# Optimization experiments

Measured on AMD Instinct MI355X. Metric: run time of the kernel, lower is better.

Reference implementation:

```python
import jax, jax.numpy as jnp
import numpy as np

B, M_IN, M_OUT, C = 4, 16, 32, 32


def setup_inputs() -> dict:
    key = jax.random.key(0)
    kx, = jax.random.split(key, 1)
    x = jax.random.normal(kx, (B, M_IN, C, C, C, C), dtype=jnp.float32)
    init = jnp.ones((M_IN, M_OUT), dtype=jnp.float32) / M_IN
    return {"x": x, "alpha": init, "beta": init, "gamma": init, "delta": init}


def reference(x, alpha, beta, gamma, delta):
    # Faithful to the torch code's permute+sum bookkeeping (note: torch's
    # permute(0,1,3,2,4,5).sum((2,4,5)) reduces ORIGINAL axes (3,4,5),
    # keeping original axis 2 -- identical to s1).
    s1 = x.sum(axis=(3, 4, 5))  # (B, M_in, C), keeps axis 2
    s2 = x.sum(axis=(3, 4, 5))  # same as s1 (permuted-sum in torch keeps axis 2)
    s3 = x.sum(axis=(2, 4, 5))  # keeps axis 3
    s4 = x.sum(axis=(2, 3, 5))  # keeps axis 4
    s = jnp.stack([s1, s2, s3, s4], axis=2)            # (B, M_in, 4, C)
    w = jnp.stack([alpha, beta, gamma, delta], axis=2)  # (M_in, M_out, 4)
    # 'bmic,mnd->bnic': sums over m and w's stack axis d; keeps s's stack axis i.
    out = jnp.einsum('bmic,mnd->bnic', s, w)            # (B, M_out, 4, C)
    return out
```

## Files before the change

### kernel.cpp

```cpp
#include <hip/hip_runtime.h>


__global__ __launch_bounds__(256) void reduce_k(const float* __restrict__ x,
                                                float* __restrict__ s3part,
                                                float* __restrict__ s4part) {
    const int t   = threadIdx.x;
    const int bid = blockIdx.x;
    const int wv  = t >> 6;
    const int g   = (t & 63) >> 3;

    __shared__ float lds3[32][33];

    const float4* xv = (const float4*)x + (size_t)bid * 8192;

    float acc4 = 0.0f;
    #pragma unroll 4
    for (int it = 0; it < 32; ++it) {
        float4 v = xv[it * 256 + t];
        float s = (v.x + v.y) + (v.z + v.w);
        s += __shfl_xor(s, 1, 64);
        s += __shfl_xor(s, 2, 64);
        s += __shfl_xor(s, 4, 64);
        acc4 += s;
        if ((t & 7) == 0) lds3[it][wv * 8 + g] = s;
    }

    if ((t & 7) == 0) s4part[bid * 32 + (t >> 3)] = acc4;

    __syncthreads();

    if (t < 32) {
        float a = 0.0f;
        #pragma unroll
        for (int k = 0; k < 32; ++k) a += lds3[t][k];
        s3part[bid * 32 + t] = a;
    }
}

__global__ __launch_bounds__(256) void finalize_k(const float* __restrict__ s3part,
                                                  const float* __restrict__ s4part,
                                                  const float* __restrict__ alpha,
                                                  const float* __restrict__ beta,
                                                  const float* __restrict__ gamma,
                                                  const float* __restrict__ delta,
                                                  float* __restrict__ out) {
    const int b = blockIdx.x;
    const int t = threadIdx.x;

    __shared__ float S1[16][32];
    __shared__ float S3[16][32];
    __shared__ float S4[16][32];
    __shared__ float W[16][32];

    #pragma unroll
    for (int i = t; i < 512; i += 256)
        W[i >> 5][i & 31] = alpha[i] + beta[i] + gamma[i] + delta[i];

    #pragma unroll
    for (int idx = t; idx < 512; idx += 256) {
        const int m = idx >> 5;
        const int c = idx & 31;
        const int bm = b * 16 + m;
        float a3 = 0.0f, a4 = 0.0f;
        #pragma unroll 4
        for (int c2 = 0; c2 < 32; ++c2) {
            a3 += s3part[(bm * 32 + c2) * 32 + c];
            a4 += s4part[(bm * 32 + c2) * 32 + c];
        }
        S3[m][c] = a3;
        S4[m][c] = a4;
        float a1 = 0.0f;
        #pragma unroll 4
        for (int k = 0; k < 32; ++k)
            a1 += s3part[(bm * 32 + c) * 32 + k];
        S1[m][c] = a1;
    }
    __syncthreads();

    #pragma unroll
    for (int idx = t; idx < 4096; idx += 256) {
        const int c = idx & 31;
        const int i = (idx >> 5) & 3;
        const int n = idx >> 7;
        const float (*S)[32] = (i <= 1) ? S1 : (i == 2 ? S3 : S4);
        float acc = 0.0f;
        #pragma unroll
        for (int m = 0; m < 16; ++m)
            acc += S[m][c] * W[m][n];
        out[((b * 32 + n) * 4 + i) * 32 + c] = acc;
    }
}

extern "C" void kernel_launch(void* const* d_in, const int* in_sizes, int n_in,
                              void* d_out, int out_size, void* d_ws, size_t ws_size,
                              hipStream_t stream) {
    const float* x     = (const float*)d_in[0];
    const float* alpha = (const float*)d_in[1];
    const float* beta  = (const float*)d_in[2];
    const float* gamma = (const float*)d_in[3];
    const float* delta = (const float*)d_in[4];
    float* out = (float*)d_out;
    float* ws  = (float*)d_ws;

    float* s3part = ws;
    float* s4part = ws + 65536;

    reduce_k<<<2048, 256, 0, stream>>>(x, s3part, s4part);
    finalize_k<<<4, 256, 0, stream>>>(s3part, s4part, alpha, beta, gamma, delta, out);
}
```

Baseline: 372.6 us.

## Replace per-iteration shuffles with LDS transpose reduction and compute s1 in reduce kernel

New measurement: 371.1 us. No clear change (-0.4%).

```diff
diff --git a/kernel.cpp b/kernel.cpp
--- a/kernel.cpp
+++ b/kernel.cpp
@@ -3,42 +3,64 @@
 
 __global__ __launch_bounds__(256) void reduce_k(const float* __restrict__ x,
                                                 float* __restrict__ s3part,
-                                                float* __restrict__ s4part) {
+                                                float* __restrict__ s4part,
+                                                float* __restrict__ s1) {
     const int t   = threadIdx.x;
     const int bid = blockIdx.x;
-    const int wv  = t >> 6;
-    const int g   = (t & 63) >> 3;
 
-    __shared__ float lds3[32][33];
+    __shared__ float l3[256][33];
+    __shared__ float red3[8][32];
+    __shared__ float lds1[4];
 
     const float4* xv = (const float4*)x + (size_t)bid * 8192;
 
-    float acc4 = 0.0f;
-    #pragma unroll 4
+    float acc = 0.0f;
+    #pragma unroll 8
     for (int it = 0; it < 32; ++it) {
         float4 v = xv[it * 256 + t];
         float s = (v.x + v.y) + (v.z + v.w);
-        s += __shfl_xor(s, 1, 64);
-        s += __shfl_xor(s, 2, 64);
-        s += __shfl_xor(s, 4, 64);
-        acc4 += s;
-        if ((t & 7) == 0) lds3[it][wv * 8 + g] = s;
+        acc += s;
+        l3[t][it] = s;
     }
 
-    if ((t & 7) == 0) s4part[bid * 32 + (t >> 3)] = acc4;
+    float g = acc;
+    g += __shfl_xor(g, 1, 64);
+    g += __shfl_xor(g, 2, 64);
+    g += __shfl_xor(g, 4, 64);
+    if ((t & 7) == 0) s4part[bid * 32 + (t >> 3)] = g;
+
+    float w = g;
+    w += __shfl_xor(w, 8, 64);
+    w += __shfl_xor(w, 16, 64);
+    w += __shfl_xor(w, 32, 64);
+    if ((t & 63) == 0) lds1[t >> 6] = w;
+
+    __syncthreads();
+
+    {
+        const int it = t & 31;
+        const int p  = t >> 5;
+        float a = 0.0f;
+        #pragma unroll
+        for (int k = 0; k < 32; ++k)
+            a += l3[p * 32 + k][it];
+        red3[p][it] = a;
+    }
+    if (t == 0)
+        s1[bid] = (lds1[0] + lds1[1]) + (lds1[2] + lds1[3]);
 
     __syncthreads();
 
     if (t < 32) {
-        float a = 0.0f;
-        #pragma unroll
-        for (int k = 0; k < 32; ++k) a += lds3[t][k];
+        float a = ((red3[0][t] + red3[1][t]) + (red3[2][t] + red3[3][t]))
+                + ((red3[4][t] + red3[5][t]) + (red3[6][t] + red3[7][t]));
         s3part[bid * 32 + t] = a;
     }
 }
 
 __global__ __launch_bounds__(256) void finalize_k(const float* __restrict__ s3part,
                                                   const float* __restrict__ s4part,
+                                                  const float* __restrict__ s1,
                                                   const float* __restrict__ alpha,
                                                   const float* __restrict__ beta,
                                                   const float* __restrict__ gamma,
@@ -47,33 +69,27 @@
     const int b = blockIdx.x;
     const int t = threadIdx.x;
 
-    __shared__ float S1[16][32];
-    __shared__ float S3[16][32];
-    __shared__ float S4[16][32];
-    __shared__ float W[16][32];
+    __shared__ float S[3][16][32];
+    __shared__ float W[512];
 
     #pragma unroll
     for (int i = t; i < 512; i += 256)
-        W[i >> 5][i & 31] = alpha[i] + beta[i] + gamma[i] + delta[i];
+        W[i] = (alpha[i] + beta[i]) + (gamma[i] + delta[i]);
 
     #pragma unroll
     for (int idx = t; idx < 512; idx += 256) {
         const int m = idx >> 5;
         const int c = idx & 31;
         const int bm = b * 16 + m;
+        S[0][m][c] = s1[bm * 32 + c];
         float a3 = 0.0f, a4 = 0.0f;
         #pragma unroll 4
         for (int c2 = 0; c2 < 32; ++c2) {
             a3 += s3part[(bm * 32 + c2) * 32 + c];
             a4 += s4part[(bm * 32 + c2) * 32 + c];
         }
-        S3[m][c] = a3;
-        S4[m][c] = a4;
-        float a1 = 0.0f;
-        #pragma unroll 4
-        for (int k = 0; k < 32; ++k)
-            a1 += s3part[(bm * 32 + c) * 32 + k];
-        S1[m][c] = a1;
+        S[1][m][c] = a3;
+        S[2][m][c] = a4;
     }
     __syncthreads();
 
@@ -82,11 +98,11 @@
         const int c = idx & 31;
         const int i = (idx >> 5) & 3;
         const int n = idx >> 7;
-        const float (*S)[32] = (i <= 1) ? S1 : (i == 2 ? S3 : S4);
+        const float (*Sp)[32] = (i <= 1) ? S[0] : (i == 2 ? S[1] : S[2]);
         float acc = 0.0f;
         #pragma unroll
         for (int m = 0; m < 16; ++m)
-            acc += S[m][c] * W[m][n];
+            acc += Sp[m][c] * W[m * 32 + n];
         out[((b * 32 + n) * 4 + i) * 32 + c] = acc;
     }
 }
@@ -104,7 +120,9 @@
 
     float* s3part = ws;
     float* s4part = ws + 65536;
+    float* s1v    = ws + 131072;
 
-    reduce_k<<<2048, 256, 0, stream>>>(x, s3part, s4part);
-    finalize_k<<<4, 256, 0, stream>>>(s3part, s4part, alpha, beta, gamma, delta, out);
+    reduce_k<<<2048, 256, 0, stream>>>(x, s3part, s4part, s1v);
+    finalize_k<<<4, 256, 0, stream>>>(s3part, s4part, s1v,
+                                      alpha, beta, gamma, delta, out);
 }
```
